# Kernel tuning notes

Measured on AMD Instinct MI355X. Metric: run time of the kernel, lower is better.

The kernel has to match this reference:

```python
import jax, jax.numpy as jnp
import numpy as np

# config
D_MODEL, D_A, D_B, R, N, D, S, D_K = 512, 256, 256, 8, 2048, 4608, 4, 64
HID = 2 * D_MODEL
U_END = D_B * R
V_END = U_END + R * D_A
B_END = V_END + D_B
LAMBDA_SHARP = 1.0
TEMPERATURE = 1.0
LN_EPS = 1e-6


def _lecun(key, shape):
    fan_in = shape[-2] if len(shape) > 1 else shape[0]
    return jax.random.normal(key, shape, dtype=jnp.float32) * (1.0 / np.sqrt(fan_in))


def setup_inputs() -> dict:
    key = jax.random.key(0)
    ks = jax.random.split(key, 12)
    return {
        'x': jax.random.normal(ks[0], (256, D_MODEL), dtype=jnp.float32),
        'pool_vectors': 0.01 * jax.random.normal(ks[1], (N, D), dtype=jnp.float32),
        'A_w0': _lecun(ks[2], (D_MODEL, HID)), 'A_b0': jnp.zeros(HID),
        'A_w1': _lecun(ks[3], (HID, D_A)), 'A_b1': jnp.zeros(D_A),
        'W_Q': _lecun(ks[4], (S, D_A, D_K)),
        'W_K': _lecun(ks[5], (S, D, D_K)),
        'aspect_logits': jnp.zeros(S),
        'tau': jnp.asarray(0.5, dtype=jnp.float32),
        'W_base': 0.01 * jax.random.normal(ks[6], (D_B, D_A), dtype=jnp.float32),
        'b_base': jnp.zeros(D_B),
        'gamma': jnp.asarray(0.1, dtype=jnp.float32),
        'ln_scale': jnp.ones(D_A), 'ln_bias': jnp.zeros(D_A),
        'B_w0': _lecun(ks[7], (D_A, HID)), 'B_b0': jnp.zeros(HID),
        'B_w1': _lecun(ks[8], (HID, D_MODEL)), 'B_b1': jnp.zeros(D_MODEL),
    }


def _forward(x, pool_vectors, A_w0, A_b0, A_w1, A_b1, W_Q, W_K, aspect_logits, tau,
             W_base, b_base, gamma, ln_scale, ln_bias, B_w0, B_b0, B_w1, B_b1):
    # Part A MLP
    h_A = jax.nn.gelu(x @ A_w0 + A_b0) @ A_w1 + A_b1                     # [b, d_A]
    # Multi-aspect retrieval
    queries = jnp.einsum('bd,adq->baq', h_A, W_Q)                        # [b, S, d_k]
    keys = jnp.einsum('np,apq->naq', pool_vectors, W_K)                  # [N, S, d_k]
    q_norm = queries / (jnp.linalg.norm(queries, axis=-1, keepdims=True) + 1e-8)
    k_norm = keys / (jnp.linalg.norm(keys, axis=-1, keepdims=True) + 1e-8)
    sims = jnp.einsum('baq,naq->bna', q_norm, k_norm)                    # [b, N, S]
    w = jax.nn.softmax(aspect_logits)
    scores = jnp.einsum('bna,a->bn', sims, w)                            # [b, N]
    g = jax.nn.sigmoid(LAMBDA_SHARP * (scores - tau))
    alpha_raw = g * jnp.exp(scores / TEMPERATURE)
    alpha = alpha_raw / (jnp.sum(alpha_raw, axis=-1, keepdims=True) + 1e-8)
    # Assemble per-sample weight matrix from low-rank factors
    U = pool_vectors[:, :U_END].reshape(N, D_B, R)
    V = pool_vectors[:, U_END:V_END].reshape(N, R, D_A)
    bias = pool_vectors[:, V_END:B_END]                                  # [N, d_B]
    UV = jnp.einsum('ndr,nre->nde', U, V)                                # [N, d_B, d_A]
    W_assembled = W_base[None] + jnp.einsum('bn,nde->bde', alpha, UV)    # [b, d_B, d_A]
    b_assembled = b_base[None] + jnp.einsum('bn,nd->bd', alpha, bias)
    # Middle layer: dynamic matmul + residual + LayerNorm
    h_t = jnp.einsum('ba,bca->bc', h_A, W_assembled) + b_assembled
    y = h_A + gamma * h_t
    mu = jnp.mean(y, axis=-1, keepdims=True)
    var = jnp.mean((y - mu) ** 2, axis=-1, keepdims=True)
    h_mid = (y - mu) / jnp.sqrt(var + LN_EPS) * ln_scale + ln_bias
    # Part B MLP
    output = jax.nn.gelu(h_mid @ B_w0 + B_b0) @ B_w1 + B_b1
    return output, alpha, W_assembled, keys


def reference(x, pool_vectors, A_w0, A_b0, A_w1, A_b1, W_Q, W_K, aspect_logits, tau,
              W_base, b_base, gamma, ln_scale, ln_bias, B_w0, B_b0, B_w1, B_b1):
    return _forward(x, pool_vectors, A_w0, A_b0, A_w1, A_b1, W_Q, W_K, aspect_logits, tau,
                    W_base, b_base, gamma, ln_scale, ln_bias, B_w0, B_b0, B_w1, B_b1)
```

## Files before the change

### kernel.cpp

```cpp
#include <hip/hip_runtime.h>
#include <hip/hip_bf16.h>
#include <math.h>

#define N_POOL 2048
#define D_POOL 4608

typedef __hip_bfloat16 bf16;
typedef __attribute__((ext_vector_type(8))) short bf16x8;
typedef __attribute__((ext_vector_type(4))) float f32x4;
typedef __attribute__((ext_vector_type(4))) unsigned short u16x4;

#define IX 0
#define IPOOL 1
#define IAW0 2
#define IAB0 3
#define IAW1 4
#define IAB1 5
#define IWQ 6
#define IWK 7
#define ILOG 8
#define ITAU 9
#define IWBASE 10
#define IBBASE 11
#define IGAMMA 12
#define ILNS 13
#define ILNB 14
#define IBW0 15
#define IBB0 16
#define IBW1 17
#define IBB1 18

__device__ inline float wsum(float v) {
#pragma unroll
    for (int off = 32; off > 0; off >>= 1) v += __shfl_xor(v, off, 64);
    return v;
}
__device__ inline float ldin(const void* p, size_t i, int f) {
    if (f) return __bfloat162float(((const bf16*)p)[i]);
    return ((const float*)p)[i];
}
__device__ inline float gelu_f(float x) {
    float t = tanhf(0.7978845608028654f * (x + 0.044715f * x * x * x));
    return 0.5f * x * (1.0f + t);
}
__device__ inline unsigned short bfbits(float f) {
    __hip_bfloat16 h = __float2bfloat16(f);
    return *reinterpret_cast<unsigned short*>(&h);
}

struct P19 { const void* p[19]; long n[19]; };

__global__ void detect_all(P19 ip, int* flags) {
    const int j = blockIdx.x;
    const unsigned short* u = (const unsigned short*)ip.p[j];
    long nelem = ip.n[j];
    long nhalf = nelem >> 1; if (nhalf < 1) nhalf = 1;
    long kstep = (nhalf + 2047) >> 11; if (kstep < 1) kstep = 1;
    int W = 0, S = 0, Z = 0, O = 0, C = 0;
    for (long k = threadIdx.x; k * kstep < nhalf; k += 256) {
        long i = k * kstep * 2;
        unsigned short ev = u[i], od = u[i + 1];
        int e = (ev >> 7) & 0xFF;
        if (ev == 0) Z++;
        else if (e >= 90 && e <= 141) S++;
        else W++;
        if (od) O++;
        C++;
    }
    __shared__ int sw[256], ss[256], sz[256], so[256], sc[256];
    sw[threadIdx.x] = W; ss[threadIdx.x] = S; sz[threadIdx.x] = Z;
    so[threadIdx.x] = O; sc[threadIdx.x] = C;
    __syncthreads();
    if (threadIdx.x == 0) {
        int tw = 0, ts = 0, tz = 0, to = 0, tc = 0;
        for (int i = 0; i < 256; i++) {
            tw += sw[i]; ts += ss[i]; tz += sz[i]; to += so[i]; tc += sc[i];
        }
        int f;
        if (tw * 16 > tc) f = 0;
        else if (ts == 0 && tw == 0) f = (to > 0) ? 0 : 1;
        else f = (ts >= tz) ? 1 : 0;
        flags[j] = f;
    }
}

template <int TRANSB>
__global__ __launch_bounds__(256) void gemm64_splitk(
    const void* __restrict__ A, int lda, int afi,
    const void* __restrict__ B, int ldb, int bfi, size_t boffs,
    float* __restrict__ C, int ldc, int KC, const int* __restrict__ flags)
{
    const int fa = (afi == -2) ? 1 : ((afi >= 0) ? flags[afi] : 0);
    const int fb = (bfi >= 0) ? flags[bfi] : 0;
    __shared__ __align__(16) float As[16][68];
    __shared__ __align__(16) float Bs[16][68];
    const int tid = threadIdx.x;
    const int tx = tid & 15, ty = tid >> 4;
    const int bx = blockIdx.x, by = blockIdx.y;
    const int kbeg = blockIdx.z * KC;
    float acc[4][4] = {};
    for (int k0 = kbeg; k0 < kbeg + KC; k0 += 16) {
#pragma unroll
        for (int i = 0; i < 4; i++) {
            int idx = tid + i * 256;
            int m = idx >> 4, kk = idx & 15;
            As[kk][m] = ldin(A, (size_t)(by * 64 + m) * lda + k0 + kk, fa);
        }
#pragma unroll
        for (int i = 0; i < 4; i++) {
            int idx = tid + i * 256;
            if (TRANSB) {
                int nn2 = idx >> 4, kk = idx & 15;
                Bs[kk][nn2] = ldin(B, boffs + (size_t)(bx * 64 + nn2) * ldb + k0 + kk, fb);
            } else {
                int kk = idx >> 6, nn2 = idx & 63;
                Bs[kk][nn2] = ldin(B, boffs + (size_t)(k0 + kk) * ldb + bx * 64 + nn2, fb);
            }
        }
        __syncthreads();
#pragma unroll
        for (int kk = 0; kk < 16; kk++) {
            float4 av4 = *(const float4*)&As[kk][ty * 4];
            float4 bv4 = *(const float4*)&Bs[kk][tx * 4];
            float av[4] = {av4.x, av4.y, av4.z, av4.w};
            float bv[4] = {bv4.x, bv4.y, bv4.z, bv4.w};
#pragma unroll
            for (int i = 0; i < 4; i++)
#pragma unroll
                for (int j = 0; j < 4; j++) acc[i][j] += av[i] * bv[j];
        }
        __syncthreads();
    }
#pragma unroll
    for (int i = 0; i < 4; i++) {
        int m = by * 64 + ty * 4 + i;
#pragma unroll
        for (int j = 0; j < 4; j++) {
            int n = bx * 64 + tx * 4 + j;
            atomicAdd(&C[(size_t)m * ldc + n], acc[i][j]);
        }
    }
}

__global__ __launch_bounds__(64) void gemm_mfma_atomic(
    const unsigned short* __restrict__ A, int lda,
    const unsigned short* __restrict__ Bmat, int ldb,
    float* __restrict__ C, int ldc, int KC)
{
    const int m0 = blockIdx.x * 32;
    const int n0 = blockIdx.y * 64;
    const unsigned short* B = Bmat + (size_t)blockIdx.y * 64 * ldb;
    const int kbeg = blockIdx.z * KC;
    const int l = threadIdx.x;
    const int q = l >> 4, l16 = l & 15;
    f32x4 acc[2][4] = {};
    for (int k0 = kbeg; k0 < kbeg + KC; k0 += 32) {
        bf16x8 afr[2], bfr[4];
#pragma unroll
        for (int mt = 0; mt < 2; mt++)
            afr[mt] = *(const bf16x8*)&A[(size_t)(m0 + mt * 16 + l16) * lda + k0 + q * 8];
#pragma unroll
        for (int nt = 0; nt < 4; nt++)
            bfr[nt] = *(const bf16x8*)&B[(size_t)(nt * 16 + l16) * ldb + k0 + q * 8];
#pragma unroll
        for (int mt = 0; mt < 2; mt++)
#pragma unroll
            for (int nt = 0; nt < 4; nt++)
                acc[mt][nt] = __builtin_amdgcn_mfma_f32_16x16x32_bf16(
                    afr[mt], bfr[nt], acc[mt][nt], 0, 0, 0);
    }
#pragma unroll
    for (int mt = 0; mt < 2; mt++)
#pragma unroll
        for (int nt = 0; nt < 4; nt++)
#pragma unroll
            for (int r = 0; r < 4; r++) {
                int m = m0 + mt * 16 + q * 4 + r;
                atomicAdd(&C[(size_t)m * ldc + n0 + nt * 16 + l16], acc[mt][nt][r]);
            }
}

template <int ACT>
__global__ __launch_bounds__(64) void gemm_mfma_fused(
    const unsigned short* __restrict__ A, int lda,
    const unsigned short* __restrict__ Bmat, int ldb,
    const void* __restrict__ bias, int bifi, const int* __restrict__ flags,
    float* __restrict__ Cf, unsigned short* __restrict__ Cbf,
    int ldc, int K)
{
    const int m0 = blockIdx.x * 32;
    const int n0 = blockIdx.y * 64;
    const unsigned short* B = Bmat + (size_t)blockIdx.y * 64 * ldb;
    const int l = threadIdx.x;
    const int q = l >> 4, l16 = l & 15;
    f32x4 acc[2][4] = {};
    for (int k0 = 0; k0 < K; k0 += 32) {
        bf16x8 afr[2], bfr[4];
#pragma unroll
        for (int mt = 0; mt < 2; mt++)
            afr[mt] = *(const bf16x8*)&A[(size_t)(m0 + mt * 16 + l16) * lda + k0 + q * 8];
#pragma unroll
        for (int nt = 0; nt < 4; nt++)
            bfr[nt] = *(const bf16x8*)&B[(size_t)(nt * 16 + l16) * ldb + k0 + q * 8];
#pragma unroll
        for (int mt = 0; mt < 2; mt++)
#pragma unroll
            for (int nt = 0; nt < 4; nt++)
                acc[mt][nt] = __builtin_amdgcn_mfma_f32_16x16x32_bf16(
                    afr[mt], bfr[nt], acc[mt][nt], 0, 0, 0);
    }
    float bv[4];
#pragma unroll
    for (int nt = 0; nt < 4; nt++)
        bv[nt] = bias ? ldin(bias, n0 + nt * 16 + l16, (bifi >= 0) ? flags[bifi] : 0) : 0.f;
#pragma unroll
    for (int mt = 0; mt < 2; mt++)
#pragma unroll
        for (int nt = 0; nt < 4; nt++)
#pragma unroll
            for (int r = 0; r < 4; r++) {
                int m = m0 + mt * 16 + q * 4 + r;
                int n = n0 + nt * 16 + l16;
                float v = acc[mt][nt][r] + bv[nt];
                if (ACT == 1) v = gelu_f(v);
                if (Cf)  Cf[(size_t)m * ldc + n] = v;
                if (Cbf) Cbf[(size_t)m * ldc + n] = bfbits(v);
            }
}

__global__ __launch_bounds__(256) void pool2bf(
    const void* __restrict__ pool, const int* __restrict__ flags,
    unsigned short* __restrict__ pb)
{
    const int fp = flags[IPOOL];
    const size_t total = (size_t)N_POOL * D_POOL;
    for (size_t i = ((size_t)blockIdx.x * 256 + threadIdx.x) * 4; i < total;
         i += (size_t)gridDim.x * 1024) {
        u16x4 o;
        if (fp == 0) {
            float4 v = *(const float4*)((const float*)pool + i);
            o[0] = bfbits(v.x); o[1] = bfbits(v.y); o[2] = bfbits(v.z); o[3] = bfbits(v.w);
        } else {
            o = *(const u16x4*)((const unsigned short*)pool + i);
        }
        *(u16x4*)&pb[i] = o;
    }
}

__global__ __launch_bounds__(256) void cvt2bf(
    const void* __restrict__ src, int fi, const int* __restrict__ flags,
    unsigned short* __restrict__ dst, int total)
{
    const int f = (fi >= 0) ? flags[fi] : 0;
    int i = (blockIdx.x * 256 + threadIdx.x) * 4;
    if (i >= total) return;
    if (f == 0) {
        float4 v = *(const float4*)((const float*)src + i);
        u16x4 o;
        o[0] = bfbits(v.x); o[1] = bfbits(v.y); o[2] = bfbits(v.z); o[3] = bfbits(v.w);
        *(u16x4*)&dst[i] = o;
    } else {
        *(u16x4*)&dst[i] = *(const u16x4*)((const unsigned short*)src + i);
    }
}

__global__ __launch_bounds__(256) void transp_bf(
    const void* __restrict__ src, int fi, const int* __restrict__ flags,
    unsigned short* __restrict__ dst, int rows, int cols)
{
    const int f = (fi >= 0) ? flags[fi] : 0;
    const size_t zoff = (size_t)blockIdx.z * rows * cols;
    const int rb = blockIdx.y * 64, cb = blockIdx.x * 64;
    __shared__ float tile[64][65];
    const int t = threadIdx.x;
    const int lr = t >> 6, lc = t & 63;
#pragma unroll
    for (int i = 0; i < 16; i++) {
        int r = i * 4 + lr;
        tile[r][lc] = ldin(src, zoff + (size_t)(rb + r) * cols + cb + lc, f);
    }
    __syncthreads();
#pragma unroll
    for (int i = 0; i < 16; i++) {
        int c = i * 4 + lr;
        dst[zoff + (size_t)(cb + c) * rows + rb + lc] = bfbits(tile[lc][c]);
    }
}

__global__ __launch_bounds__(256) void wk2bfT(
    const void* __restrict__ W_K, const int* __restrict__ flags,
    unsigned short* __restrict__ out)
{
    const int fk = flags[IWK];
    const int a = blockIdx.y, kb = blockIdx.x, t = threadIdx.x;
#pragma unroll
    for (int i = 0; i < 16; i++) {
        int idx = i * 256 + t;
        int kk = idx >> 6, qq = idx & 63;
        float v = ldin(W_K, (size_t)a * 294912 + (size_t)(kb * 64 + kk) * 64 + qq, fk);
        out[(size_t)(a * 64 + qq) * 4608 + kb * 64 + kk] = bfbits(v);
    }
}

__global__ __launch_bounds__(256) void bias2bfT(
    const void* __restrict__ pool, const int* __restrict__ flags,
    unsigned short* __restrict__ out)
{
    const int fp = flags[IPOOL];
    const int nb = blockIdx.x, cb = blockIdx.y, t = threadIdx.x;
#pragma unroll
    for (int i = 0; i < 16; i++) {
        int idx = i * 256 + t;
        int nn = idx >> 6, cc = idx & 63;
        float v = ldin(pool, (size_t)(nb * 64 + nn) * 4608 + 4096 + cb * 64 + cc, fp);
        out[(size_t)(cb * 64 + cc) * 2048 + nb * 64 + nn] = bfbits(v);
    }
}

__global__ __launch_bounds__(256) void init_bias_kernel(
    float* __restrict__ C, const void* __restrict__ bias, int bifi,
    const int* __restrict__ flags, int N, int total)
{
    int i = blockIdx.x * 256 + threadIdx.x;
    if (i >= total) return;
    float v = 0.f;
    if (bias) v = ldin(bias, i % N, (bifi >= 0) ? flags[bifi] : 0);
    C[i] = v;
}

__global__ __launch_bounds__(256) void knorm_kernel(
    const float* __restrict__ keys, unsigned short* __restrict__ knbf)
{
    const int n = blockIdx.x;
    const int a = threadIdx.x >> 6, q = threadIdx.x & 63;
    float v = keys[(size_t)n * 256 + a * 64 + q];
    float ss = wsum(v * v);
    knbf[(size_t)n * 256 + a * 64 + q] = bfbits(v / (sqrtf(ss) + 1e-8f));
}

__global__ __launch_bounds__(256) void qnorm_kernel(
    const float* __restrict__ qraw, const float* __restrict__ w,
    unsigned short* __restrict__ qwbf)
{
    const int b = blockIdx.x;
    const int a = threadIdx.x >> 6, q = threadIdx.x & 63;
    float v = qraw[b * 256 + a * 64 + q];
    float ss = wsum(v * v);
    qwbf[b * 256 + a * 64 + q] = bfbits(v / (sqrtf(ss) + 1e-8f) * w[a]);
}

__global__ void softmax4_kernel(const void* __restrict__ logits,
                                const int* __restrict__ flags, float* __restrict__ w) {
    if (threadIdx.x == 0) {
        int f = flags[ILOG];
        float l0 = ldin(logits, 0, f), l1 = ldin(logits, 1, f);
        float l2 = ldin(logits, 2, f), l3 = ldin(logits, 3, f);
        float m = fmaxf(fmaxf(l0, l1), fmaxf(l2, l3));
        float e0 = expf(l0 - m), e1 = expf(l1 - m), e2 = expf(l2 - m), e3 = expf(l3 - m);
        float s = e0 + e1 + e2 + e3;
        w[0] = e0 / s; w[1] = e1 / s; w[2] = e2 / s; w[3] = e3 / s;
    }
}

__global__ __launch_bounds__(256) void alpha_kernel(
    const float* __restrict__ scores, const void* __restrict__ tau_p,
    const int* __restrict__ flags,
    float* __restrict__ alpha_out, unsigned short* __restrict__ alphaT,
    unsigned short* __restrict__ alphaB)
{
    const int b = blockIdx.x;
    const int tid = threadIdx.x;
    const float tauv = ldin(tau_p, 0, flags[ITAU]);
    float ar[8];
    float lsum = 0.f;
#pragma unroll
    for (int i = 0; i < 8; i++) {
        int n = i * 256 + tid;
        float s = scores[b * 2048 + n];
        float g = 1.f / (1.f + expf(-(s - tauv)));
        ar[i] = g * expf(s);
        lsum += ar[i];
    }
    __shared__ float sb[4];
    float wsv = wsum(lsum);
    if ((tid & 63) == 0) sb[tid >> 6] = wsv;
    __syncthreads();
    float tot = sb[0] + sb[1] + sb[2] + sb[3];
    float inv = 1.f / (tot + 1e-8f);
#pragma unroll
    for (int i = 0; i < 8; i++) {
        int n = i * 256 + tid;
        float al = ar[i] * inv;
        alpha_out[b * 2048 + n] = al;
        unsigned short bb = bfbits(al);
        alphaT[(size_t)(n >> 3) * 2048 + b * 8 + (n & 7)] = bb;
        alphaB[(size_t)b * 2048 + n] = bb;
    }
}

#define QW 520
__global__ __launch_bounds__(256, 2) void assemble_mfma(
    const unsigned short* __restrict__ alphaT,
    const void* __restrict__ pool,
    const void* __restrict__ W_base,
    const int* __restrict__ flags,
    float* __restrict__ Wout)
{
    const int fp = flags[IPOOL], fw = flags[IWBASE];
    const int lid = blockIdx.x;
    const int xcd = lid & 7, idx = lid >> 3;
    const int dt = idx & 31;
    const int et = ((idx >> 5) << 3) + xcd;
    const int d0 = dt * 8, e0 = et * 16;
    const int t = threadIdx.x;
    const int w = t >> 6, l = t & 63;
    const int q = l >> 4, l16 = l & 15;

    const int nl  = t >> 3;
    const int sub = t & 7;
    const int dlp = sub >> 1;
    const int eh  = sub & 1;
    const int jj  = nl & 7;

    __shared__ __align__(16) float Us[2][32][76];
    __shared__ __align__(16) float Vs[2][32][132];
    __shared__ __align__(16) unsigned short uvb[8][QW];

    const float4* pool4 = (const float4*)pool;

    f32x4 acc[4][8] = {};

    auto load_stage = [&](int n0, float4* st) {
#pragma unroll
        for (int i = 0; i < 2; i++) {
            int f = i * 256 + t;
            int n = n0 + (f >> 4);
            int q4 = f & 15;
            if (fp == 0) {
                st[i] = pool4[(size_t)n * 1152 + d0 * 2 + q4];
            } else {
                size_t base = (size_t)n * 4608 + (size_t)d0 * 8 + q4 * 4;
                st[i] = make_float4(ldin(pool, base, 1), ldin(pool, base + 1, 1),
                                    ldin(pool, base + 2, 1), ldin(pool, base + 3, 1));
            }
        }
#pragma unroll
        for (int i = 0; i < 4; i++) {
            int f = i * 256 + t;
            int n = n0 + (f >> 5);
            int r = (f & 31) >> 2, e4 = f & 3;
            if (fp == 0) {
                st[2 + i] = pool4[(size_t)n * 1152 + 512 + r * 64 + (e0 >> 2) + e4];
            } else {
                size_t base = (size_t)n * 4608 + 2048 + (size_t)r * 256 + e0 + e4 * 4;
                st[2 + i] = make_float4(ldin(pool, base, 1), ldin(pool, base + 1, 1),
                                        ldin(pool, base + 2, 1), ldin(pool, base + 3, 1));
            }
        }
    };
    auto store_stage = [&](int bp, const float4* st) {
#pragma unroll
        for (int i = 0; i < 2; i++) {
            int f = i * 256 + t;
            *(float4*)&Us[bp][f >> 4][(f & 15) * 4] = st[i];
        }
#pragma unroll
        for (int i = 0; i < 4; i++) {
            int f = i * 256 + t;
            int r = (f & 31) >> 2, e4 = f & 3;
            *(float4*)&Vs[bp][f >> 5][r * 16 + e4 * 4] = st[2 + i];
        }
    };

    {
        float4 st[6];
        load_stage(0, st);
        store_stage(0, st);
    }
    __syncthreads();

    int p = 0;
    for (int step = 0; step < 64; step++) {
        const int n0 = step * 32;
        float4 stn[6];
        if (step < 63) load_stage(n0 + 32, stn);

        bf16x8 afr[4];
#pragma unroll
        for (int mt = 0; mt < 4; mt++) {
            const unsigned short* ap =
                alphaT + (size_t)(step * 4 + q) * 2048 + (w * 64 + mt * 16 + l16) * 8;
            afr[mt] = *(const bf16x8*)ap;
        }

        {
            const float* Ur = &Us[p][nl][dlp * 16];
            float4 Ua = *(const float4*)(Ur);
            float4 Ub = *(const float4*)(Ur + 4);
            float4 Uc = *(const float4*)(Ur + 8);
            float4 Ud = *(const float4*)(Ur + 12);
            float U0[8] = {Ua.x, Ua.y, Ua.z, Ua.w, Ub.x, Ub.y, Ub.z, Ub.w};
            float U1[8] = {Uc.x, Uc.y, Uc.z, Uc.w, Ud.x, Ud.y, Ud.z, Ud.w};
            float uv0[8] = {0.f, 0.f, 0.f, 0.f, 0.f, 0.f, 0.f, 0.f};
            float uv1[8] = {0.f, 0.f, 0.f, 0.f, 0.f, 0.f, 0.f, 0.f};
#pragma unroll
            for (int r = 0; r < 8; r++) {
                float4 va = *(const float4*)&Vs[p][nl][r * 16 + eh * 8];
                float4 vb = *(const float4*)&Vs[p][nl][r * 16 + eh * 8 + 4];
                uv0[0] += U0[r] * va.x; uv0[1] += U0[r] * va.y;
                uv0[2] += U0[r] * va.z; uv0[3] += U0[r] * va.w;
                uv0[4] += U0[r] * vb.x; uv0[5] += U0[r] * vb.y;
                uv0[6] += U0[r] * vb.z; uv0[7] += U0[r] * vb.w;
                uv1[0] += U1[r] * va.x; uv1[1] += U1[r] * va.y;
                uv1[2] += U1[r] * va.z; uv1[3] += U1[r] * va.w;
                uv1[4] += U1[r] * vb.x; uv1[5] += U1[r] * vb.y;
                uv1[6] += U1[r] * vb.z; uv1[7] += U1[r] * vb.w;
            }
            const int cg0 = dlp * 2, cg1 = cg0 + 1;
            const int wbase = w * 128 + eh * 64 + jj;
#pragma unroll
            for (int i = 0; i < 8; i++) {
                uvb[cg0][wbase + i * 8] = bfbits(uv0[i]);
                uvb[cg1][wbase + i * 8] = bfbits(uv1[i]);
            }
        }
        __syncthreads();

        bf16x8 bfr[8];
#pragma unroll
        for (int cg = 0; cg < 8; cg++)
            bfr[cg] = *(const bf16x8*)&uvb[cg][l * 8];
        if (step < 63) store_stage(p ^ 1, stn);
#pragma unroll
        for (int mt = 0; mt < 4; mt++)
#pragma unroll
            for (int cg = 0; cg < 8; cg++)
                acc[mt][cg] = __builtin_amdgcn_mfma_f32_16x16x32_bf16(
                    afr[mt], bfr[cg], acc[mt][cg], 0, 0, 0);
        __syncthreads();
        p ^= 1;
    }

    float wb[8];
#pragma unroll
    for (int cg = 0; cg < 8; cg++)
        wb[cg] = ldin(W_base, (size_t)(d0 + cg) * 256 + e0 + l16, fw);
#pragma unroll
    for (int mt = 0; mt < 4; mt++) {
#pragma unroll
        for (int cg = 0; cg < 8; cg++) {
            size_t col = (size_t)(d0 + cg) * 256 + e0 + l16;
#pragma unroll
            for (int r = 0; r < 4; r++) {
                int b = w * 64 + mt * 16 + q * 4 + r;
                Wout[(size_t)b * 65536 + col] = acc[mt][cg][r] + wb[cg];
            }
        }
    }
}

__global__ __launch_bounds__(256) void hty_kernel(
    const float* __restrict__ Wout, const float* __restrict__ hA,
    const float* __restrict__ bass, const void* __restrict__ gamma_p,
    const int* __restrict__ flags, float* __restrict__ y)
{
    const int b = blockIdx.y;
    const int c = blockIdx.x * 4 + (threadIdx.x >> 6);
    const int lane = threadIdx.x & 63;
    const float4 wv = ((const float4*)(Wout + ((size_t)b * 65536 + c * 256)))[lane];
    const float4 h4 = ((const float4*)(hA + b * 256))[lane];
    float s = wv.x * h4.x + wv.y * h4.y + wv.z * h4.z + wv.w * h4.w;
    s = wsum(s);
    if (lane == 0) {
        float ht = s + bass[b * 256 + c];
        y[b * 256 + c] = hA[b * 256 + c] + ldin(gamma_p, 0, flags[IGAMMA]) * ht;
    }
}

__global__ __launch_bounds__(256) void ln_kernel(
    const float* __restrict__ y, const void* __restrict__ ln_scale,
    const void* __restrict__ ln_bias, const int* __restrict__ flags,
    unsigned short* __restrict__ hmidbf)
{
    const int fs = flags[ILNS], fb = flags[ILNB];
    const int b = blockIdx.x, tid = threadIdx.x;
    float v = y[b * 256 + tid];
    __shared__ float s1b[4], s2b[4];
    float w1 = wsum(v), w2 = wsum(v * v);
    if ((tid & 63) == 0) { s1b[tid >> 6] = w1; s2b[tid >> 6] = w2; }
    __syncthreads();
    float mu = (s1b[0] + s1b[1] + s1b[2] + s1b[3]) * (1.f / 256.f);
    float ex2 = (s2b[0] + s2b[1] + s2b[2] + s2b[3]) * (1.f / 256.f);
    float var = ex2 - mu * mu;
    float inv = 1.f / sqrtf(var + 1e-6f);
    float hm = (v - mu) * inv * ldin(ln_scale, tid, fs) + ldin(ln_bias, tid, fb);
    hmidbf[b * 256 + tid] = bfbits(hm);
}

extern "C" void kernel_launch(void* const* d_in, const int* in_sizes, int n_in,
                              void* d_out, int out_size, void* d_ws, size_t ws_size,
                              hipStream_t stream)
{
    (void)out_size; (void)n_in;
    const void* x      = d_in[0];
    const void* pool   = d_in[1];
    const void* A_w0   = d_in[2];
    const void* A_b0   = d_in[3];
    const void* A_w1   = d_in[4];
    const void* A_b1   = d_in[5];
    const void* W_Q    = d_in[6];
    const void* W_K    = d_in[7];
    const void* logits = d_in[8];
    const void* tau    = d_in[9];
    const void* W_base = d_in[10];
    const void* b_base = d_in[11];
    const void* gamma  = d_in[12];
    const void* ln_s   = d_in[13];
    const void* ln_b   = d_in[14];
    const void* B_w0   = d_in[15];
    const void* B_b0   = d_in[16];
    const void* B_w1   = d_in[17];
    const void* B_b1   = d_in[18];

    float* out       = (float*)d_out;
    float* out0      = out;
    float* out_alpha = out + 131072;
    float* out_W     = out + 655360;
    float* out_keys  = out + 17432576;

    float* ws = (float*)d_ws;
    int*   flagp   = (int*)d_ws;
    float* ws_w    = ws + 32;
    float* ws_hA   = ws + 64;
    float* ws_bass = ws + 131136;
    float* ws_y    = ws + 196672;
    unsigned short* hmidbf = (unsigned short*)(ws + 262208);
    unsigned short* alpha_bf = (unsigned short*)(ws + 327744);

    size_t wsf = ws_size / 4;
    bool full = wsf >= 1638464;
    float* slotA;
    float* slotB;
    float* Treg;
    float* scr = (float*)out_W;
    if (full) {
        slotA = ws + 589888;
        slotB = ws + 1114176;
        Treg  = ws + 589888;
    } else {
        slotA = scr;
        slotB = scr + 524288;
        Treg  = ws + 327744;
    }
    float* scores = slotA;
    unsigned short* knbf = (unsigned short*)slotB;
    unsigned short* T1bf = (unsigned short*)Treg;
    unsigned short* bw0T = (unsigned short*)(Treg + 131072);

    unsigned short* xbf    = (unsigned short*)(scr + 1048576);
    unsigned short* aw0T   = (unsigned short*)(scr + 1114112);
    unsigned short* aw1T   = (unsigned short*)(scr + 1376256);
    unsigned short* wqT    = (unsigned short*)(scr + 1507328);
    unsigned short* Gbf    = (unsigned short*)(scr + 1540096);
    unsigned short* hAbf   = (unsigned short*)(scr + 1671168);
    float*          qraw   = scr + 1703936;
    unsigned short* qwbf   = (unsigned short*)(scr + 1769472);
    unsigned short* poolbf = (unsigned short*)(scr + 2097152);
    unsigned short* wkbT   = (unsigned short*)(scr + 7340032);
    unsigned short* biasT  = (unsigned short*)(scr + 8388608);
    unsigned short* alphaB = (unsigned short*)(scr + 8912896);

    P19 ip;
    for (int i = 0; i < 19; i++) { ip.p[i] = d_in[i]; ip.n[i] = in_sizes[i]; }
    detect_all<<<19, 256, 0, stream>>>(ip, flagp);
    softmax4_kernel<<<1, 64, 0, stream>>>(logits, flagp, ws_w);
    pool2bf<<<2048, 256, 0, stream>>>(pool, flagp, poolbf);
    wk2bfT<<<dim3(72, 4), 256, 0, stream>>>(W_K, flagp, wkbT);
    bias2bfT<<<dim3(32, 4), 256, 0, stream>>>(pool, flagp, biasT);
    cvt2bf<<<128, 256, 0, stream>>>(x, IX, flagp, xbf, 131072);
    transp_bf<<<dim3(16, 8, 1), 256, 0, stream>>>(A_w0, IAW0, flagp, aw0T, 512, 1024);
    transp_bf<<<dim3(4, 16, 1), 256, 0, stream>>>(A_w1, IAW1, flagp, aw1T, 1024, 256);
    transp_bf<<<dim3(1, 4, 4), 256, 0, stream>>>(W_Q, IWQ, flagp, wqT, 256, 64);
    gemm_mfma_fused<1><<<dim3(8, 16), 64, 0, stream>>>(
        xbf, 512, aw0T, 512, A_b0, IAB0, flagp, nullptr, Gbf, 1024, 512);
    gemm_mfma_fused<0><<<dim3(8, 4), 64, 0, stream>>>(
        Gbf, 1024, aw1T, 1024, A_b1, IAB1, flagp, ws_hA, hAbf, 256, 1024);
    init_bias_kernel<<<2048, 256, 0, stream>>>(out_keys, nullptr, -1, flagp, 256, 524288);
    gemm_mfma_atomic<<<dim3(64, 4, 8), 64, 0, stream>>>(
        poolbf, 4608, wkbT, 4608, out_keys, 256, 576);
    knorm_kernel<<<2048, 256, 0, stream>>>(out_keys, knbf);
    gemm_mfma_fused<0><<<dim3(8, 4), 64, 0, stream>>>(
        hAbf, 256, wqT, 256, nullptr, -1, flagp, qraw, nullptr, 256, 256);
    qnorm_kernel<<<256, 256, 0, stream>>>(qraw, ws_w, qwbf);
    gemm_mfma_fused<0><<<dim3(8, 32), 64, 0, stream>>>(
        qwbf, 256, knbf, 256, nullptr, -1, flagp, scores, nullptr, 2048, 256);
    alpha_kernel<<<256, 256, 0, stream>>>(scores, tau, flagp, out_alpha, alpha_bf, alphaB);
    init_bias_kernel<<<256, 256, 0, stream>>>(ws_bass, b_base, IBBASE, flagp, 256, 65536);
    gemm_mfma_atomic<<<dim3(8, 4, 8), 64, 0, stream>>>(
        alphaB, 2048, biasT, 2048, ws_bass, 256, 256);
    assemble_mfma<<<512, 256, 0, stream>>>(alpha_bf, pool, W_base, flagp, out_W);
    transp_bf<<<dim3(16, 4, 1), 256, 0, stream>>>(B_w0, IBW0, flagp, bw0T, 256, 1024);
    hty_kernel<<<dim3(64, 256), 256, 0, stream>>>(out_W, ws_hA, ws_bass, gamma, flagp, ws_y);
    ln_kernel<<<256, 256, 0, stream>>>(ws_y, ln_s, ln_b, flagp, hmidbf);
    gemm_mfma_fused<1><<<dim3(8, 16), 64, 0, stream>>>(
        hmidbf, 256, bw0T, 256, B_b0, IBB0, flagp, nullptr, T1bf, 1024, 256);
    init_bias_kernel<<<512, 256, 0, stream>>>(out0, B_b1, IBB1, flagp, 512, 131072);
    gemm64_splitk<0><<<dim3(8, 4, 4), 256, 0, stream>>>(
        T1bf, 1024, -2, B_w1, 512, IBW1, 0,
        out0, 512, 256, flagp);
}
```

Baseline: 514.0 us.

## Fuse dynamic matvec into assemble epilogue and fuse query norm into GEMM

Computes the per-row h_A·W_assembled partial dot products inside the assemble kernel's epilogue, reducing across lanes with shuffles and atomically adding into a y partial buffer. This removes the separate hty pass that re-read the full 64 MB W_assembled output. Residual and gamma are folded into the LayerNorm kernel. The query projection also gets a dedicated MFMA kernel that normalizes and weights queries in its epilogue, dropping the qnorm launch. The cost is extra shuffles and atomics in the assemble epilogue, plus one more zero-init launch.

After: 565.1 us. 9.9% more time.

```diff
diff --git a/kernel.cpp b/kernel.cpp
--- a/kernel.cpp
+++ b/kernel.cpp
@@ -228,6 +228,55 @@
             }
 }
 
+__global__ __launch_bounds__(64) void queries_mfma(
+    const unsigned short* __restrict__ hAbf,
+    const unsigned short* __restrict__ wqT,
+    const float* __restrict__ w,
+    unsigned short* __restrict__ qwbf)
+{
+    const int m0 = blockIdx.x * 32;
+    const int a  = blockIdx.y;
+    const unsigned short* B = wqT + (size_t)a * 64 * 256;
+    const int l = threadIdx.x;
+    const int q = l >> 4, l16 = l & 15;
+    f32x4 acc[2][4] = {};
+    for (int k0 = 0; k0 < 256; k0 += 32) {
+        bf16x8 afr[2], bfr[4];
+#pragma unroll
+        for (int mt = 0; mt < 2; mt++)
+            afr[mt] = *(const bf16x8*)&hAbf[(size_t)(m0 + mt * 16 + l16) * 256 + k0 + q * 8];
+#pragma unroll
+        for (int nt = 0; nt < 4; nt++)
+            bfr[nt] = *(const bf16x8*)&B[(size_t)(nt * 16 + l16) * 256 + k0 + q * 8];
+#pragma unroll
+        for (int mt = 0; mt < 2; mt++)
+#pragma unroll
+            for (int nt = 0; nt < 4; nt++)
+                acc[mt][nt] = __builtin_amdgcn_mfma_f32_16x16x32_bf16(
+                    afr[mt], bfr[nt], acc[mt][nt], 0, 0, 0);
+    }
+    const float wa = w[a];
+#pragma unroll
+    for (int mt = 0; mt < 2; mt++) {
+#pragma unroll
+        for (int r = 0; r < 4; r++) {
+            float ss = 0.f;
+#pragma unroll
+            for (int nt = 0; nt < 4; nt++) {
+                float v = acc[mt][nt][r];
+                ss += v * v;
+            }
+            ss += __shfl_xor(ss, 1, 64); ss += __shfl_xor(ss, 2, 64);
+            ss += __shfl_xor(ss, 4, 64); ss += __shfl_xor(ss, 8, 64);
+            float inv = wa / (sqrtf(ss) + 1e-8f);
+            int b = m0 + mt * 16 + q * 4 + r;
+#pragma unroll
+            for (int nt = 0; nt < 4; nt++)
+                qwbf[(size_t)b * 256 + a * 64 + nt * 16 + l16] = bfbits(acc[mt][nt][r] * inv);
+        }
+    }
+}
+
 __global__ __launch_bounds__(256) void pool2bf(
     const void* __restrict__ pool, const int* __restrict__ flags,
     unsigned short* __restrict__ pb)
@@ -338,17 +387,6 @@
     knbf[(size_t)n * 256 + a * 64 + q] = bfbits(v / (sqrtf(ss) + 1e-8f));
 }
 
-__global__ __launch_bounds__(256) void qnorm_kernel(
-    const float* __restrict__ qraw, const float* __restrict__ w,
-    unsigned short* __restrict__ qwbf)
-{
-    const int b = blockIdx.x;
-    const int a = threadIdx.x >> 6, q = threadIdx.x & 63;
-    float v = qraw[b * 256 + a * 64 + q];
-    float ss = wsum(v * v);
-    qwbf[b * 256 + a * 64 + q] = bfbits(v / (sqrtf(ss) + 1e-8f) * w[a]);
-}
-
 __global__ void softmax4_kernel(const void* __restrict__ logits,
                                 const int* __restrict__ flags, float* __restrict__ w) {
     if (threadIdx.x == 0) {
@@ -404,7 +442,9 @@
     const void* __restrict__ pool,
     const void* __restrict__ W_base,
     const int* __restrict__ flags,
-    float* __restrict__ Wout)
+    float* __restrict__ Wout,
+    const float* __restrict__ hA,
+    float* __restrict__ ypart)
 {
     const int fp = flags[IPOOL], fw = flags[IWBASE];
     const int lid = blockIdx.x;
@@ -545,6 +585,14 @@
 #pragma unroll
     for (int cg = 0; cg < 8; cg++)
         wb[cg] = ldin(W_base, (size_t)(d0 + cg) * 256 + e0 + l16, fw);
+
+    float ha[4][4];
+#pragma unroll
+    for (int mt = 0; mt < 4; mt++)
+#pragma unroll
+        for (int r = 0; r < 4; r++)
+            ha[mt][r] = hA[(size_t)(w * 64 + mt * 16 + q * 4 + r) * 256 + e0 + l16];
+
 #pragma unroll
     for (int mt = 0; mt < 4; mt++) {
 #pragma unroll
@@ -553,38 +601,29 @@
 #pragma unroll
             for (int r = 0; r < 4; r++) {
                 int b = w * 64 + mt * 16 + q * 4 + r;
-                Wout[(size_t)b * 65536 + col] = acc[mt][cg][r] + wb[cg];
-            }
-        }
-    }
-}
-
-__global__ __launch_bounds__(256) void hty_kernel(
-    const float* __restrict__ Wout, const float* __restrict__ hA,
+                float v = acc[mt][cg][r] + wb[cg];
+                Wout[(size_t)b * 65536 + col] = v;
+                float pp = v * ha[mt][r];
+                pp += __shfl_xor(pp, 1, 64); pp += __shfl_xor(pp, 2, 64);
+                pp += __shfl_xor(pp, 4, 64); pp += __shfl_xor(pp, 8, 64);
+                if (l16 == 0)
+                    atomicAdd(&ypart[(size_t)b * 256 + d0 + cg], pp);
+            }
+        }
+    }
+}
+
+__global__ __launch_bounds__(256) void ln_kernel(
+    const float* __restrict__ hA, const float* __restrict__ ypart,
     const float* __restrict__ bass, const void* __restrict__ gamma_p,
-    const int* __restrict__ flags, float* __restrict__ y)
-{
-    const int b = blockIdx.y;
-    const int c = blockIdx.x * 4 + (threadIdx.x >> 6);
-    const int lane = threadIdx.x & 63;
-    const float4 wv = ((const float4*)(Wout + ((size_t)b * 65536 + c * 256)))[lane];
-    const float4 h4 = ((const float4*)(hA + b * 256))[lane];
-    float s = wv.x * h4.x + wv.y * h4.y + wv.z * h4.z + wv.w * h4.w;
-    s = wsum(s);
-    if (lane == 0) {
-        float ht = s + bass[b * 256 + c];
-        y[b * 256 + c] = hA[b * 256 + c] + ldin(gamma_p, 0, flags[IGAMMA]) * ht;
-    }
-}
-
-__global__ __launch_bounds__(256) void ln_kernel(
-    const float* __restrict__ y, const void* __restrict__ ln_scale,
-    const void* __restrict__ ln_bias, const int* __restrict__ flags,
-    unsigned short* __restrict__ hmidbf)
+    const void* __restrict__ ln_scale, const void* __restrict__ ln_bias,
+    const int* __restrict__ flags, unsigned short* __restrict__ hmidbf)
 {
     const int fs = flags[ILNS], fb = flags[ILNB];
     const int b = blockIdx.x, tid = threadIdx.x;
-    float v = y[b * 256 + tid];
+    const int i = b * 256 + tid;
+    float gm = ldin(gamma_p, 0, flags[IGAMMA]);
+    float v = hA[i] + gm * (ypart[i] + bass[i]);
     __shared__ float s1b[4], s2b[4];
     float w1 = wsum(v), w2 = wsum(v * v);
     if ((tid & 63) == 0) { s1b[tid >> 6] = w1; s2b[tid >> 6] = w2; }
@@ -633,7 +672,7 @@
     float* ws_w    = ws + 32;
     float* ws_hA   = ws + 64;
     float* ws_bass = ws + 131136;
-    float* ws_y    = ws + 196672;
+    float* ypart   = ws + 196672;
     unsigned short* hmidbf = (unsigned short*)(ws + 262208);
     unsigned short* alpha_bf = (unsigned short*)(ws + 327744);
 
@@ -663,7 +702,6 @@
     unsigned short* wqT    = (unsigned short*)(scr + 1507328);
     unsigned short* Gbf    = (unsigned short*)(scr + 1540096);
     unsigned short* hAbf   = (unsigned short*)(scr + 1671168);
-    float*          qraw   = scr + 1703936;
     unsigned short* qwbf   = (unsigned short*)(scr + 1769472);
     unsigned short* poolbf = (unsigned short*)(scr + 2097152);
     unsigned short* wkbT   = (unsigned short*)(scr + 7340032);
@@ -689,19 +727,19 @@
     gemm_mfma_atomic<<<dim3(64, 4, 8), 64, 0, stream>>>(
         poolbf, 4608, wkbT, 4608, out_keys, 256, 576);
     knorm_kernel<<<2048, 256, 0, stream>>>(out_keys, knbf);
-    gemm_mfma_fused<0><<<dim3(8, 4), 64, 0, stream>>>(
-        hAbf, 256, wqT, 256, nullptr, -1, flagp, qraw, nullptr, 256, 256);
-    qnorm_kernel<<<256, 256, 0, stream>>>(qraw, ws_w, qwbf);
+    queries_mfma<<<dim3(8, 4), 64, 0, stream>>>(hAbf, wqT, ws_w, qwbf);
     gemm_mfma_fused<0><<<dim3(8, 32), 64, 0, stream>>>(
         qwbf, 256, knbf, 256, nullptr, -1, flagp, scores, nullptr, 2048, 256);
     alpha_kernel<<<256, 256, 0, stream>>>(scores, tau, flagp, out_alpha, alpha_bf, alphaB);
     init_bias_kernel<<<256, 256, 0, stream>>>(ws_bass, b_base, IBBASE, flagp, 256, 65536);
     gemm_mfma_atomic<<<dim3(8, 4, 8), 64, 0, stream>>>(
         alphaB, 2048, biasT, 2048, ws_bass, 256, 256);
-    assemble_mfma<<<512, 256, 0, stream>>>(alpha_bf, pool, W_base, flagp, out_W);
+    init_bias_kernel<<<256, 256, 0, stream>>>(ypart, nullptr, -1, flagp, 256, 65536);
+    assemble_mfma<<<512, 256, 0, stream>>>(alpha_bf, pool, W_base, flagp,
+                                           out_W, ws_hA, ypart);
     transp_bf<<<dim3(16, 4, 1), 256, 0, stream>>>(B_w0, IBW0, flagp, bw0T, 256, 1024);
-    hty_kernel<<<dim3(64, 256), 256, 0, stream>>>(out_W, ws_hA, ws_bass, gamma, flagp, ws_y);
-    ln_kernel<<<256, 256, 0, stream>>>(ws_y, ln_s, ln_b, flagp, hmidbf);
+    ln_kernel<<<256, 256, 0, stream>>>(ws_hA, ypart, ws_bass, gamma,
+                                       ln_s, ln_b, flagp, hmidbf);
     gemm_mfma_fused<1><<<dim3(8, 16), 64, 0, stream>>>(
         hmidbf, 256, bw0T, 256, B_b0, IBB0, flagp, nullptr, T1bf, 1024, 256);
     init_bias_kernel<<<512, 256, 0, stream>>>(out0, B_b1, IBB1, flagp, 512, 131072);
```
